# Performance work log

Measured on AMD Instinct MI355X. Metric: run time of the kernel, lower is better.

The kernel has to match this reference:

```python
import jax, jax.numpy as jnp
import numpy as np

D_MODEL = 1024
NHEAD = 16
HEAD_DIM = D_MODEL // NHEAD
B, S = 8, 1024
NEG = -1e9  # finite stand-in for -inf (same softmax result, grad-safe)


def setup_inputs() -> dict:
    key = jax.random.key(0)
    ks = jax.random.split(key, 12)
    sc = 1.0 / np.sqrt(D_MODEL)
    inp = {
        "q": jax.random.normal(ks[0], (B, S, D_MODEL), jnp.float32),
        "k": jax.random.normal(ks[1], (B, S, D_MODEL), jnp.float32),
        "v": jax.random.normal(ks[2], (B, S, D_MODEL), jnp.float32),
        "padding_mask": jax.random.bernoulli(ks[3], 0.1, (B, S)),
        "causal_mask": jnp.where(jnp.tril(jnp.ones((S, S), bool)), 0.0, NEG).astype(jnp.float32),
        "wq": jax.random.normal(ks[4], (D_MODEL, D_MODEL), jnp.float32) * sc,
        "bq": jax.random.normal(ks[5], (D_MODEL,), jnp.float32) * sc,
        "wk": jax.random.normal(ks[6], (D_MODEL, D_MODEL), jnp.float32) * sc,
        "wv": jax.random.normal(ks[7], (D_MODEL, D_MODEL), jnp.float32) * sc,
        "bv": jax.random.normal(ks[8], (D_MODEL,), jnp.float32) * sc,
        "wo": jax.random.normal(ks[9], (D_MODEL, D_MODEL), jnp.float32) * sc,
        "bo": jax.random.normal(ks[10], (D_MODEL,), jnp.float32) * sc,
    }
    return inp


def reference(q, k, v, padding_mask, causal_mask, wq, bq, wk, wv, bv, wo, bo):
    b = q.shape[0]
    # projections (torch Linear: x @ W.T + b); k_linear has no bias
    qp = q @ wq.T + bq
    kp = k @ wk.T
    vp = v @ wv.T + bv
    # [B, S, H, Dh] -> [B, H, S, Dh]
    qh = qp.reshape(b, -1, NHEAD, HEAD_DIM).transpose(0, 2, 1, 3)
    kh = kp.reshape(b, -1, NHEAD, HEAD_DIM).transpose(0, 2, 1, 3)
    vh = vp.reshape(b, -1, NHEAD, HEAD_DIM).transpose(0, 2, 1, 3)
    scores = jnp.einsum("bhqd,bhkd->bhqk", qh, kh) / np.sqrt(HEAD_DIM).astype(np.float32)
    scores = jnp.where(padding_mask[:, None, None, :], NEG, scores)
    scores = scores + causal_mask[None, None, :, :]
    attn = jax.nn.softmax(scores, axis=-1)
    out = jnp.einsum("bhqk,bhkd->bhqd", attn, vh)
    out = out.transpose(0, 2, 1, 3).reshape(b, -1, D_MODEL)
    return out @ wo.T + bo
```

## Files before the change

### kernel.cpp

```cpp
#include <hip/hip_runtime.h>
#include <hip/hip_bf16.h>
#include <cstdint>
#include <math.h>


typedef __bf16 bf16_t;
typedef __bf16 bf16x8 __attribute__((ext_vector_type(8)));
typedef __bf16 bf16x4 __attribute__((ext_vector_type(4)));
typedef float  f32x4  __attribute__((ext_vector_type(4)));

#define MFMA16(a, b, c) __builtin_amdgcn_mfma_f32_16x16x32_bf16((a), (b), (c), 0, 0, 0)
#define NEGV (-1e9f)

__device__ __forceinline__ void gl_lds16(const void* gp, void* lp) {
  __builtin_amdgcn_global_load_lds(
      (__attribute__((address_space(1))) void*)(gp),
      (__attribute__((address_space(3))) void*)(lp), 16, 0, 0);
}

__device__ __forceinline__ unsigned int pk2(float lo, float hi) {
  unsigned short a = __builtin_bit_cast(unsigned short, (bf16_t)lo);
  unsigned short b = __builtin_bit_cast(unsigned short, (bf16_t)hi);
  return (unsigned int)a | ((unsigned int)b << 16);
}

__device__ __forceinline__ void cvt_body(const float* __restrict__ in,
                                         bf16_t* __restrict__ out, int i, int n8) {
  if (i < n8) {
    const float4* p = reinterpret_cast<const float4*>(in) + (size_t)i * 2;
    float4 a = p[0], b = p[1];
    bf16x8 r = {(bf16_t)a.x, (bf16_t)a.y, (bf16_t)a.z, (bf16_t)a.w,
                (bf16_t)b.x, (bf16_t)b.y, (bf16_t)b.z, (bf16_t)b.w};
    *reinterpret_cast<bf16x8*>(out + (size_t)i * 8) = r;
  }
}

__global__ __launch_bounds__(256) void cvt_qkv(const float* __restrict__ a, const float* __restrict__ b,
                                               const float* __restrict__ c,
                                               bf16_t* __restrict__ oa, bf16_t* __restrict__ ob,
                                               bf16_t* __restrict__ oc, int n8) {
  const float* in = blockIdx.y == 0 ? a : (blockIdx.y == 1 ? b : c);
  bf16_t* out     = blockIdx.y == 0 ? oa : (blockIdx.y == 1 ? ob : oc);
  cvt_body(in, out, blockIdx.x * 256 + threadIdx.x, n8);
}

__global__ __launch_bounds__(256) void cvt_w4(const float* __restrict__ a, const float* __restrict__ b,
                                              const float* __restrict__ c, const float* __restrict__ d,
                                              bf16_t* __restrict__ oa, bf16_t* __restrict__ ob,
                                              bf16_t* __restrict__ oc, bf16_t* __restrict__ od, int n8) {
  const float* in = blockIdx.y == 0 ? a : (blockIdx.y == 1 ? b : (blockIdx.y == 2 ? c : d));
  bf16_t* out     = blockIdx.y == 0 ? oa : (blockIdx.y == 1 ? ob : (blockIdx.y == 2 ? oc : od));
  cvt_body(in, out, blockIdx.x * 256 + threadIdx.x, n8);
}

__device__ __forceinline__ void panel_decode(int r, int& bx, int& by) {
  const int t8 = r >> 3;
  bx = t8 & 7;
  by = ((t8 >> 3) << 3) | (r & 7);
}

__global__ __launch_bounds__(256) void gemm_qkv(const bf16_t* __restrict__ qbf,
                                                const bf16_t* __restrict__ kbf,
                                                const bf16_t* __restrict__ vbf,
                                                const bf16_t* __restrict__ wqb,
                                                const bf16_t* __restrict__ wkb,
                                                const bf16_t* __restrict__ wvb,
                                                const float* __restrict__ bq,
                                                const float* __restrict__ bv,
                                                bf16_t* __restrict__ qp,
                                                bf16_t* __restrict__ kp,
                                                bf16_t* __restrict__ vtw) {
  __shared__ bf16_t As[128 * 32];
  __shared__ bf16_t Bs[128 * 32];
  const int z = blockIdx.y;
  const bf16_t* A = z == 0 ? qbf : (z == 1 ? kbf : vbf);
  const bf16_t* W = z == 0 ? wqb : (z == 1 ? wkb : wvb);
  const int t = threadIdx.x;
  const int w = t >> 6, l = t & 63, lr = l & 15, lg = l >> 4;
  int bx, by;
  panel_decode((int)blockIdx.x, bx, by);
  const int m0 = by * 128, n0 = bx * 128;
  const int wm = (w >> 1) * 64, wn = (w & 1) * 64;
  const int K = 1024, N = 1024;

  f32x4 acc[4][4] = {};
  const bf16_t* Ag = A + (size_t)(m0 + (t >> 2)) * K + (t & 3) * 8;
  const bf16_t* Wg = W + (size_t)(n0 + (t >> 2)) * K + (t & 3) * 8;
  char* AsB = (char*)As;
  char* BsB = (char*)Bs;

  for (int kt = 0; kt < K; kt += 32) {
    gl_lds16(Ag + kt,                    AsB + t * 16);
    gl_lds16(Ag + kt + (size_t)64 * K,   AsB + 4096 + t * 16);
    gl_lds16(Wg + kt,                    BsB + t * 16);
    gl_lds16(Wg + kt + (size_t)64 * K,   BsB + 4096 + t * 16);
    asm volatile("s_waitcnt vmcnt(0)");
    __syncthreads();

    bf16x8 af[4], bfr[4];
#pragma unroll
    for (int mt = 0; mt < 4; mt++)
      af[mt] = *reinterpret_cast<const bf16x8*>(AsB + ((wm + mt * 16 + lr) * 32 + lg * 8) * 2);
#pragma unroll
    for (int nt = 0; nt < 4; nt++)
      bfr[nt] = *reinterpret_cast<const bf16x8*>(BsB + ((wn + nt * 16 + lr) * 32 + lg * 8) * 2);
#pragma unroll
    for (int mt = 0; mt < 4; mt++)
#pragma unroll
      for (int nt = 0; nt < 4; nt++)
        acc[mt][nt] = MFMA16(af[mt], bfr[nt], acc[mt][nt]);
    __syncthreads();
  }

#pragma unroll
  for (int nt = 0; nt < 4; nt++) {
    const int col = n0 + wn + nt * 16 + lr;
    const float bb = (z == 0) ? bq[col] : (z == 2 ? bv[col] : 0.0f);
#pragma unroll
    for (int mt = 0; mt < 4; mt++) {
#pragma unroll
      for (int i = 0; i < 4; i++) {
        const int row = m0 + wm + mt * 16 + lg * 4 + i;
        const float v = acc[mt][nt][i] + bb;
        if (z == 0) {
          qp[(size_t)row * N + col] = (bf16_t)(v * 0.125f);
        } else if (z == 1) {
          kp[(size_t)row * N + col] = (bf16_t)v;
        } else {
          const int b = row >> 10, s = row & 1023;
          const int h = col >> 6, d = col & 63;
          vtw[(size_t)((b * 16 + h) * 64 + d) * 1024 + s] = (bf16_t)v;
        }
      }
    }
  }
}

__global__ __launch_bounds__(256) void gemm_out(const bf16_t* __restrict__ A,
                                                const bf16_t* __restrict__ W,
                                                const float* __restrict__ bias,
                                                float* __restrict__ outp) {
  __shared__ bf16_t As[128 * 32];
  __shared__ bf16_t Bs[128 * 32];
  const int t = threadIdx.x;
  const int w = t >> 6, l = t & 63, lr = l & 15, lg = l >> 4;
  int bx, by;
  panel_decode((int)blockIdx.x, bx, by);
  const int m0 = by * 128, n0 = bx * 128;
  const int wm = (w >> 1) * 64, wn = (w & 1) * 64;
  const int K = 1024, N = 1024;

  f32x4 acc[4][4] = {};
  const bf16_t* Ag = A + (size_t)(m0 + (t >> 2)) * K + (t & 3) * 8;
  const bf16_t* Wg = W + (size_t)(n0 + (t >> 2)) * K + (t & 3) * 8;
  char* AsB = (char*)As;
  char* BsB = (char*)Bs;

  for (int kt = 0; kt < K; kt += 32) {
    gl_lds16(Ag + kt,                    AsB + t * 16);
    gl_lds16(Ag + kt + (size_t)64 * K,   AsB + 4096 + t * 16);
    gl_lds16(Wg + kt,                    BsB + t * 16);
    gl_lds16(Wg + kt + (size_t)64 * K,   BsB + 4096 + t * 16);
    asm volatile("s_waitcnt vmcnt(0)");
    __syncthreads();

    bf16x8 af[4], bfr[4];
#pragma unroll
    for (int mt = 0; mt < 4; mt++)
      af[mt] = *reinterpret_cast<const bf16x8*>(AsB + ((wm + mt * 16 + lr) * 32 + lg * 8) * 2);
#pragma unroll
    for (int nt = 0; nt < 4; nt++)
      bfr[nt] = *reinterpret_cast<const bf16x8*>(BsB + ((wn + nt * 16 + lr) * 32 + lg * 8) * 2);
#pragma unroll
    for (int mt = 0; mt < 4; mt++)
#pragma unroll
      for (int nt = 0; nt < 4; nt++)
        acc[mt][nt] = MFMA16(af[mt], bfr[nt], acc[mt][nt]);
    __syncthreads();
  }

#pragma unroll
  for (int nt = 0; nt < 4; nt++) {
    const int col = n0 + wn + nt * 16 + lr;
    const float bb = bias[col];
#pragma unroll
    for (int mt = 0; mt < 4; mt++)
#pragma unroll
      for (int i = 0; i < 4; i++) {
        const int row = m0 + wm + mt * 16 + lg * 4 + i;
        outp[(size_t)row * N + col] = acc[mt][nt][i] + bb;
      }
  }
}

__device__ __forceinline__ void pack_bfly(const f32x4 (&s)[4], int lg,
                                          bf16x8& pbv0, bf16x8& pbv1) {
  unsigned int u[4][2], sh[4][2];
#pragma unroll
  for (int nt = 0; nt < 4; nt++) {
    u[nt][0] = pk2(s[nt][0], s[nt][1]);
    u[nt][1] = pk2(s[nt][2], s[nt][3]);
  }
#pragma unroll
  for (int nt = 0; nt < 4; nt++) {
    sh[nt][0] = (unsigned int)__shfl_xor((int)u[nt][0], 16, 64);
    sh[nt][1] = (unsigned int)__shfl_xor((int)u[nt][1], 16, 64);
  }
  const bool ev = (lg & 1) == 0;
  unsigned int Y[8];
  Y[0] = ev ? u[0][0] : sh[1][0];  Y[1] = ev ? u[0][1] : sh[1][1];
  Y[2] = ev ? u[2][0] : sh[3][0];  Y[3] = ev ? u[2][1] : sh[3][1];
  Y[4] = ev ? sh[0][0] : u[1][0];  Y[5] = ev ? sh[0][1] : u[1][1];
  Y[6] = ev ? sh[2][0] : u[3][0];  Y[7] = ev ? sh[2][1] : u[3][1];
  const bool mid = (lg == 1) || (lg == 2);
#pragma unroll
  for (int j = 0; j < 8; j++) {
    const unsigned int z = (unsigned int)__shfl_xor((int)Y[j], 48, 64);
    Y[j] = mid ? z : Y[j];
  }
  union U8 { unsigned int u[4]; bf16x8 v; };
  U8 p0, p1;
  p0.u[0] = Y[0]; p0.u[1] = Y[1]; p0.u[2] = Y[4]; p0.u[3] = Y[5];
  p1.u[0] = Y[2]; p1.u[1] = Y[3]; p1.u[2] = Y[6]; p1.u[3] = Y[7];
  pbv0 = p0.v;
  pbv1 = p1.v;
}

__global__ __launch_bounds__(512, 8) void attn_fused(const bf16_t* __restrict__ qp,
                                                     const bf16_t* __restrict__ kp,
                                                     const bf16_t* __restrict__ vt,
                                                     const int* __restrict__ pad,
                                                     bf16_t* __restrict__ outp) {
  __shared__ bf16_t Ks[2][64 * 64];
  __shared__ bf16_t Vts[2][64 * 64];
  __shared__ int padI[1024];
  __shared__ int sfl[8], sfh[8];
  const int t = threadIdx.x, w = t >> 6, l = t & 63, lr = l & 15, lg = l >> 4;
  const int L = (int)blockIdx.x;
  const int bh = (L & 7) + ((L >> 6) << 3);
  const int j = (L >> 3) & 7;
  const int b = bh >> 4, h = bh & 15;
  const int lo = j, hi = 15 - j;

  const int srow = t >> 3, sc = t & 7;
  const int gc = sc ^ (srow & 7);
  const bf16_t* kgb = kp + (size_t)(b * 1024 + srow) * 1024 + h * 64 + gc * 8;
  const bf16_t* vgb = vt + (size_t)(bh * 64 + srow) * 1024 + gc * 8;

  auto stage = [&](int bufi, int k0s) {
    gl_lds16(kgb + (size_t)k0s * 1024, (char*)(Ks[bufi]) + t * 16);
    gl_lds16(vgb + k0s,                (char*)(Vts[bufi]) + t * 16);
  };

  bool unl = false, unh = false;
  for (int jj = t; jj <= hi * 64; jj += 512) {
    const bool u = (pad[b * 1024 + jj] == 0);
    unh |= u;
    unl |= (u && (jj <= lo * 64));
  }
  const bool al = __any(unl), ah = __any(unh);
  if (l == 0) { sfl[w] = al ? 1 : 0; sfh[w] = ah ? 1 : 0; }

  stage(0, 0);
  if (t < 256) gl_lds16(pad + b * 1024 + t * 4, (char*)padI + t * 16);

  const int mytile = (w < 4) ? hi : lo;
  const int qrow_l = mytile * 64 + (w & 3) * 16 + lr;
  const int base16 = mytile * 64 + (w & 3) * 16;
  const bf16_t* qg = qp + (size_t)(b * 1024 + qrow_l) * 1024 + h * 64 + lg * 8;
  const bf16x8 qa0 = *reinterpret_cast<const bf16x8*>(qg);
  const bf16x8 qa1 = *reinterpret_cast<const bf16x8*>(qg + 32);

  __syncthreads();
  int ul = 0, uh = 0;
#pragma unroll
  for (int i = 0; i < 8; i++) { ul |= sfl[i]; uh |= sfh[i]; }
  const bool mydeg = (w < 4) ? (uh == 0) : (ul == 0);
  const int ktEnd = (ul == 0) ? 16 : (hi + 1);

  f32x4 o[4] = {};
  float m_ = -INFINITY, ld_ = 0.0f;

  for (int kt = 0; kt < ktEnd; ++kt) {
    const int cur = kt & 1;
    if (kt + 1 < ktEnd) {
      stage(cur ^ 1, (kt + 1) * 64);
      asm volatile("s_waitcnt vmcnt(2)" ::: "memory");
    } else {
      asm volatile("s_waitcnt vmcnt(0)" ::: "memory");
    }
    __builtin_amdgcn_s_barrier();

    if (kt <= mytile || mydeg) {
      const char* Kb = (const char*)(Ks[cur]);
      const char* Vb = (const char*)(Vts[cur]);
      const int k0 = kt * 64;

      f32x4 s[4] = {};
#pragma unroll
      for (int nt = 0; nt < 4; nt++) {
        const int row = nt * 16 + lr;
        const int sw = (row & 7) << 4;
        bf16x8 kb0 = *reinterpret_cast<const bf16x8*>(Kb + row * 128 + ((lg * 16) ^ sw));
        bf16x8 kb1 = *reinterpret_cast<const bf16x8*>(Kb + row * 128 + ((lg * 16 + 64) ^ sw));
        s[nt] = MFMA16(kb0, qa0, s[nt]);
        s[nt] = MFMA16(kb1, qa1, s[nt]);
      }

      const bool nc = (k0 + 63 > base16);
#pragma unroll
      for (int nt = 0; nt < 4; nt++) {
        const int kc4 = k0 + nt * 16 + lg * 4;
        const int4 pd = *reinterpret_cast<const int4*>(&padI[kc4]);
        const int pdv[4] = {pd.x, pd.y, pd.z, pd.w};
#pragma unroll
        for (int i = 0; i < 4; i++) {
          float v = s[nt][i];
          if (pdv[i]) v = NEGV;
          if (nc && (kc4 + i > qrow_l)) v += NEGV;
          s[nt][i] = v;
        }
      }

      float mx = s[0][0];
#pragma unroll
      for (int nt = 0; nt < 4; nt++)
#pragma unroll
        for (int i = 0; i < 4; i++) mx = fmaxf(mx, s[nt][i]);
      mx = fmaxf(mx, __shfl_xor(mx, 16, 64));
      mx = fmaxf(mx, __shfl_xor(mx, 32, 64));

      if (!__all(mx <= m_ - 88.0f)) {
        if (!__all(mx <= m_ + 8.0f)) {
          const float mn = fmaxf(m_, mx);
          const float scl = __expf(m_ - mn);
          m_ = mn;
          ld_ *= scl;
#pragma unroll
          for (int nt = 0; nt < 4; nt++) o[nt] *= scl;
        }
        float a = 0.0f;
#pragma unroll
        for (int nt = 0; nt < 4; nt++)
#pragma unroll
          for (int i = 0; i < 4; i++) {
            const float p = __expf(s[nt][i] - m_);
            s[nt][i] = p;
            a += p;
          }
        a += __shfl_xor(a, 16, 64);
        a += __shfl_xor(a, 32, 64);
        ld_ += a;

        bf16x8 pb0, pb1;
        pack_bfly(s, lg, pb0, pb1);

#pragma unroll
        for (int nt = 0; nt < 4; nt++) {
          const int vrow = nt * 16 + lr;
          const int vsw = (vrow & 7) << 4;
          bf16x8 vf0 = *reinterpret_cast<const bf16x8*>(Vb + vrow * 128 + ((lg * 16) ^ vsw));
          bf16x8 vf1 = *reinterpret_cast<const bf16x8*>(Vb + vrow * 128 + ((64 + lg * 16) ^ vsw));
          o[nt] = MFMA16(vf0, pb0, o[nt]);
          o[nt] = MFMA16(vf1, pb1, o[nt]);
        }
      }
    }
    __builtin_amdgcn_s_barrier();
  }

  const float rinv = 1.0f / ld_;
#pragma unroll
  for (int nt = 0; nt < 4; nt++) {
    bf16x4 r = {(bf16_t)(o[nt][0] * rinv), (bf16_t)(o[nt][1] * rinv),
                (bf16_t)(o[nt][2] * rinv), (bf16_t)(o[nt][3] * rinv)};
    *reinterpret_cast<bf16x4*>(outp + (size_t)(b * 1024 + qrow_l) * 1024 + h * 64 + nt * 16 + lg * 4) = r;
  }
}

extern "C" void kernel_launch(void* const* d_in, const int* in_sizes, int n_in,
                              void* d_out, int out_size, void* d_ws, size_t ws_size,
                              hipStream_t stream) {
  const float* q   = (const float*)d_in[0];
  const float* k   = (const float*)d_in[1];
  const float* v   = (const float*)d_in[2];
  const int*   pad = (const int*)d_in[3];
  const float* wq  = (const float*)d_in[5];
  const float* bq  = (const float*)d_in[6];
  const float* wk  = (const float*)d_in[7];
  const float* wv  = (const float*)d_in[8];
  const float* bv  = (const float*)d_in[9];
  const float* wo  = (const float*)d_in[10];
  const float* bo  = (const float*)d_in[11];

  const int M = 8192, N = 1024;
  const int nBig = M * N;
  const int nW   = N * 1024;

  char* ws = (char*)d_ws;
  const size_t MiB = 1024 * 1024;
  bf16_t* qbf = (bf16_t*)(ws + 0 * MiB);
  bf16_t* kbf = (bf16_t*)(ws + 16 * MiB);
  bf16_t* vbf = (bf16_t*)(ws + 32 * MiB);
  bf16_t* qp  = (bf16_t*)(ws + 48 * MiB);
  bf16_t* kp  = (bf16_t*)(ws + 64 * MiB);
  bf16_t* vtw = (bf16_t*)(ws + 80 * MiB);
  bf16_t* wqb = (bf16_t*)(ws + 96 * MiB);
  bf16_t* wkb = (bf16_t*)(ws + 98 * MiB);
  bf16_t* wvb = (bf16_t*)(ws + 100 * MiB);
  bf16_t* wob = (bf16_t*)(ws + 102 * MiB);
  bf16_t* attnO = qbf;

  cvt_qkv<<<dim3(nBig / 2048, 3), 256, 0, stream>>>(q, k, v, qbf, kbf, vbf, nBig / 8);
  cvt_w4 <<<dim3(nW / 2048, 4), 256, 0, stream>>>(wq, wk, wv, wo, wqb, wkb, wvb, wob, nW / 8);

  gemm_qkv<<<dim3(512, 3), 256, 0, stream>>>(qbf, kbf, vbf, wqb, wkb, wvb, bq, bv, qp, kp, vtw);

  attn_fused<<<1024, 512, 0, stream>>>(qp, kp, vtw, pad, attnO);

  gemm_out<<<512, 256, 0, stream>>>(attnO, wob, bo, (float*)d_out);
}
```

Measured before the change: 201.5 us.

## Double-buffer GEMM LDS tiles and stage V transpose through shared memory

```diff
diff --git a/kernel.cpp b/kernel.cpp
--- a/kernel.cpp
+++ b/kernel.cpp
@@ -70,8 +70,7 @@
                                                 bf16_t* __restrict__ qp,
                                                 bf16_t* __restrict__ kp,
                                                 bf16_t* __restrict__ vtw) {
-  __shared__ bf16_t As[128 * 32];
-  __shared__ bf16_t Bs[128 * 32];
+  __shared__ bf16_t smem[4][128 * 32];
   const int z = blockIdx.y;
   const bf16_t* A = z == 0 ? qbf : (z == 1 ? kbf : vbf);
   const bf16_t* W = z == 0 ? wqb : (z == 1 ? wkb : wvb);
@@ -86,17 +85,23 @@
   f32x4 acc[4][4] = {};
   const bf16_t* Ag = A + (size_t)(m0 + (t >> 2)) * K + (t & 3) * 8;
   const bf16_t* Wg = W + (size_t)(n0 + (t >> 2)) * K + (t & 3) * 8;
-  char* AsB = (char*)As;
-  char* BsB = (char*)Bs;
-
-  for (int kt = 0; kt < K; kt += 32) {
-    gl_lds16(Ag + kt,                    AsB + t * 16);
-    gl_lds16(Ag + kt + (size_t)64 * K,   AsB + 4096 + t * 16);
-    gl_lds16(Wg + kt,                    BsB + t * 16);
-    gl_lds16(Wg + kt + (size_t)64 * K,   BsB + 4096 + t * 16);
-    asm volatile("s_waitcnt vmcnt(0)");
-    __syncthreads();
-
+
+  auto stage = [&](int buf, int kt) {
+    gl_lds16(Ag + kt,                  (char*)(smem[buf])     + t * 16);
+    gl_lds16(Ag + kt + (size_t)64 * K, (char*)(smem[buf])     + 4096 + t * 16);
+    gl_lds16(Wg + kt,                  (char*)(smem[2 + buf]) + t * 16);
+    gl_lds16(Wg + kt + (size_t)64 * K, (char*)(smem[2 + buf]) + 4096 + t * 16);
+  };
+
+  stage(0, 0);
+  __syncthreads();
+
+  for (int it = 0; it < 32; ++it) {
+    const int cur = it & 1;
+    if (it < 31) stage(cur ^ 1, (it + 1) * 32);
+
+    const char* AsB = (const char*)(smem[cur]);
+    const char* BsB = (const char*)(smem[2 + cur]);
     bf16x8 af[4], bfr[4];
 #pragma unroll
     for (int mt = 0; mt < 4; mt++)
@@ -112,26 +117,47 @@
     __syncthreads();
   }
 
-#pragma unroll
-  for (int nt = 0; nt < 4; nt++) {
-    const int col = n0 + wn + nt * 16 + lr;
-    const float bb = (z == 0) ? bq[col] : (z == 2 ? bv[col] : 0.0f);
-#pragma unroll
-    for (int mt = 0; mt < 4; mt++) {
-#pragma unroll
-      for (int i = 0; i < 4; i++) {
-        const int row = m0 + wm + mt * 16 + lg * 4 + i;
-        const float v = acc[mt][nt][i] + bb;
-        if (z == 0) {
-          qp[(size_t)row * N + col] = (bf16_t)(v * 0.125f);
-        } else if (z == 1) {
-          kp[(size_t)row * N + col] = (bf16_t)v;
-        } else {
-          const int b = row >> 10, s = row & 1023;
-          const int h = col >> 6, d = col & 63;
-          vtw[(size_t)((b * 16 + h) * 64 + d) * 1024 + s] = (bf16_t)v;
+  if (z != 2) {
+    bf16_t* outp = (z == 0) ? qp : kp;
+    const float sc = (z == 0) ? 0.125f : 1.0f;
+#pragma unroll
+    for (int nt = 0; nt < 4; nt++) {
+      const int col = n0 + wn + nt * 16 + lr;
+      const float bb = (z == 0) ? bq[col] : 0.0f;
+#pragma unroll
+      for (int mt = 0; mt < 4; mt++)
+#pragma unroll
+        for (int i = 0; i < 4; i++) {
+          const int row = m0 + wm + mt * 16 + lg * 4 + i;
+          outp[(size_t)row * N + col] = (bf16_t)((acc[mt][nt][i] + bb) * sc);
         }
-      }
+    }
+  } else {
+    char* T = (char*)smem;
+#pragma unroll
+    for (int nt = 0; nt < 4; nt++) {
+      const int col_l = wn + nt * 16 + lr;
+      const float bb = bv[n0 + col_l];
+#pragma unroll
+      for (int mt = 0; mt < 4; mt++)
+#pragma unroll
+        for (int i = 0; i < 4; i++) {
+          const int row_l = wm + mt * 16 + lg * 4 + i;
+          *(bf16_t*)(T + col_l * 256 + ((row_l * 2) ^ ((col_l & 7) << 4))) =
+              (bf16_t)(acc[mt][nt][i] + bb);
+        }
+    }
+    __syncthreads();
+    const int b = m0 >> 10, s0 = m0 & 1023;
+    const int c_l = t >> 1, half = t & 1;
+    bf16_t* dst = vtw + (size_t)(b * 1024 + n0 + c_l) * 1024 + s0 + half * 64;
+    const char* Trow = T + c_l * 256;
+    const int sw = c_l & 7;
+#pragma unroll
+    for (int jj = 0; jj < 8; jj++) {
+      const int lc = half * 8 + jj;
+      bf16x8 vv = *reinterpret_cast<const bf16x8*>(Trow + ((lc ^ sw) << 4));
+      *reinterpret_cast<bf16x8*>(dst + jj * 8) = vv;
     }
   }
 }
@@ -140,8 +166,7 @@
                                                 const bf16_t* __restrict__ W,
                                                 const float* __restrict__ bias,
                                                 float* __restrict__ outp) {
-  __shared__ bf16_t As[128 * 32];
-  __shared__ bf16_t Bs[128 * 32];
+  __shared__ bf16_t smem[4][128 * 32];
   const int t = threadIdx.x;
   const int w = t >> 6, l = t & 63, lr = l & 15, lg = l >> 4;
   int bx, by;
@@ -153,17 +178,23 @@
   f32x4 acc[4][4] = {};
   const bf16_t* Ag = A + (size_t)(m0 + (t >> 2)) * K + (t & 3) * 8;
   const bf16_t* Wg = W + (size_t)(n0 + (t >> 2)) * K + (t & 3) * 8;
-  char* AsB = (char*)As;
-  char* BsB = (char*)Bs;
-
-  for (int kt = 0; kt < K; kt += 32) {
-    gl_lds16(Ag + kt,                    AsB + t * 16);
-    gl_lds16(Ag + kt + (size_t)64 * K,   AsB + 4096 + t * 16);
-    gl_lds16(Wg + kt,                    BsB + t * 16);
-    gl_lds16(Wg + kt + (size_t)64 * K,   BsB + 4096 + t * 16);
-    asm volatile("s_waitcnt vmcnt(0)");
-    __syncthreads();
-
+
+  auto stage = [&](int buf, int kt) {
+    gl_lds16(Ag + kt,                  (char*)(smem[buf])     + t * 16);
+    gl_lds16(Ag + kt + (size_t)64 * K, (char*)(smem[buf])     + 4096 + t * 16);
+    gl_lds16(Wg + kt,                  (char*)(smem[2 + buf]) + t * 16);
+    gl_lds16(Wg + kt + (size_t)64 * K, (char*)(smem[2 + buf]) + 4096 + t * 16);
+  };
+
+  stage(0, 0);
+  __syncthreads();
+
+  for (int it = 0; it < 32; ++it) {
+    const int cur = it & 1;
+    if (it < 31) stage(cur ^ 1, (it + 1) * 32);
+
+    const char* AsB = (const char*)(smem[cur]);
+    const char* BsB = (const char*)(smem[2 + cur]);
     bf16x8 af[4], bfr[4];
 #pragma unroll
     for (int mt = 0; mt < 4; mt++)
```

Result: faster. 189.8 us (-5.8%).
